# Optimization experiments

Measured on AMD Instinct MI355X. Metric: run time of the kernel, lower is better.

The kernel has to match this reference:

```python
import jax, jax.numpy as jnp
import numpy as np

EPS = 1e-5

def _bn_relu_over_batch(x, gamma, beta):
    # x: [..., B, F] where batch axis is -2; per-step training-mode BatchNorm1d
    mu = x.mean(axis=-2, keepdims=True)
    var = ((x - mu) ** 2).mean(axis=-2, keepdims=True)  # biased var (torch BN)
    xn = (x - mu) * jax.lax.rsqrt(var + EPS)
    return jax.nn.relu(xn * gamma + beta)

def setup_inputs() -> dict:
    key = jax.random.key(0)
    ks = jax.random.split(key, 8)
    B, T, D_in, E, C, D_out = 8192, 128, 2, 128, 128, 5
    s = 0.1
    return {
        "inputs": jax.random.normal(ks[0], (B, T, D_in), jnp.float32),
        "W_emb": jax.random.normal(ks[1], (E, D_in), jnp.float32) * s,
        "b_emb": jnp.zeros((E,), jnp.float32),
        "g_emb": jnp.ones((E,), jnp.float32),
        "be_emb": jnp.zeros((E,), jnp.float32),
        "W_ih": jax.random.normal(ks[2], (4 * C, E), jnp.float32) * s,
        "W_hh": jax.random.normal(ks[3], (4 * C, C), jnp.float32) * s,
        "b_ih": jnp.zeros((4 * C,), jnp.float32),
        "b_hh": jnp.zeros((4 * C,), jnp.float32),
        "W_out": jax.random.normal(ks[4], (D_out, C), jnp.float32) * s,
        "b_out": jnp.zeros((D_out,), jnp.float32),
        "g_out": jnp.ones((D_out,), jnp.float32),
        "be_out": jnp.zeros((D_out,), jnp.float32),
    }

def reference(inputs, W_emb, b_emb, g_emb, be_emb, W_ih, W_hh, b_ih, b_hh,
              W_out, b_out, g_out, be_out):
    B, T, _ = inputs.shape
    C = W_hh.shape[1]
    # Input embedding: Linear + per-step BatchNorm (batch stats) + ReLU, vectorized over T
    x = jnp.einsum('btd,ed->bte', inputs, W_emb) + b_emb      # [B,T,E]
    x = jnp.transpose(x, (1, 0, 2))                           # [T,B,E]
    x = _bn_relu_over_batch(x, g_emb, be_emb)                 # BN over batch per step

    def step(carry, xt):
        h, c = carry
        gates = xt @ W_ih.T + b_ih + h @ W_hh.T + b_hh        # [B,4C]
        i, f, g, o = jnp.split(gates, 4, axis=-1)             # torch LSTMCell order
        i = jax.nn.sigmoid(i); f = jax.nn.sigmoid(f)
        g = jnp.tanh(g); o = jax.nn.sigmoid(o)
        c = f * c + i * g
        h = o * jnp.tanh(c)
        return (h, c), h

    h0 = jnp.zeros((B, C), inputs.dtype)
    _, h_all = jax.lax.scan(step, (h0, h0), x)                # [T,B,C]

    # Output embedding: Linear + per-step BatchNorm + ReLU
    y = jnp.einsum('tbc,oc->tbo', h_all, W_out) + b_out       # [T,B,5]
    y = _bn_relu_over_batch(y, g_out, be_out)
    return jnp.transpose(y, (1, 0, 2))                        # [B,T,5]
```

## Files before the change

kernel.cpp:

```cpp
#include <hip/hip_runtime.h>

typedef __attribute__((ext_vector_type(8))) short short8;
typedef __attribute__((ext_vector_type(4))) float floatx4;

#define B_TOT 8192
#define T_STEPS 128
#define E_DIM 128
#define C_DIM 128
#define D_OUT 5
#define BN_EPS 1e-5f

#define LOG2E 1.4426950408889634f
#define TWO_LOG2E 2.8853900817779268f

#define WS_WCAT   0u
#define WS_WOUT   (WS_WCAT + 262144u)
#define WS_A0     (WS_WOUT + 4096u)
#define WS_A1     (WS_A0 + 65536u)
#define WS_CC     (WS_A1 + 65536u)
#define WS_STATS  (WS_CC + 65536u)
#define WS_PART   (WS_STATS + 5120u)
#define WS_Y      (WS_PART + 20480u)

__device__ __forceinline__ float bf2f(unsigned short h){
  return __uint_as_float(((unsigned int)h) << 16);
}
__device__ __forceinline__ unsigned short f2b(float v){
  unsigned int u = __float_as_uint(v);
  u += 0x7FFFu + ((u >> 16) & 1u);
  return (unsigned short)(u >> 16);
}
__device__ __forceinline__ unsigned short f2b_fast(float v){
  return (unsigned short)((__float_as_uint(v) + 0x8000u) >> 16);
}
__device__ __forceinline__ float ldf(const void* p, int i, int bf){
  return bf ? bf2f(((const unsigned short*)p)[i]) : ((const float*)p)[i];
}
__device__ __forceinline__ int sniff_bf(const void* ones){
  return *(const unsigned int*)ones == 0x3F803F80u;
}

__global__ void k_prep_mom(const void* W_ih, const void* W_hh, const void* W_out,
                           unsigned short* wcat, unsigned short* wout,
                           const void* x, float* part, const void* ones){
  const int bf = sniff_bf(ones);
  const int tid = threadIdx.x;
  if (blockIdx.x < 260){
    int i = blockIdx.x * 512 + tid;
    if (i < 512*256){
      int n = i >> 8, k = i & 255;
      float v = (k < 128) ? ldf(W_ih, n*128 + k, bf) : ldf(W_hh, n*128 + (k-128), bf);
      float sc = ((n >> 7) == 2) ? TWO_LOG2E : -LOG2E;
      wcat[i] = f2b(v * sc);
    } else {
      int j = i - 512*256;
      int n = j >> 7, k = j & 127;
      float v = (n < D_OUT) ? ldf(W_out, n*128 + k, bf) : 0.0f;
      wout[j] = f2b(v);
    }
    return;
  }
  const int mb  = blockIdx.x - 260;
  const int wdw = (mb >> 3) * 8;
  const int rg  = mb & 7;
  const int wv = tid >> 6, lane = tid & 63;
  __shared__ float red[8][16][3];

  if (!bf){
    const float* xp = (const float*)x;
    const int row_b = tid >> 4, j = tid & 15;
    float a0=0, a1=0, a2=0;
    for (int c = 0; c < 32; ++c){
      int row = rg*1024 + c*32 + row_b;
      float v = xp[row*256 + wdw*2 + j];
      float p = __shfl_xor(v, 1, 64);
      if ((j & 1) == 0){ a0 += v; a1 += v*v; a2 += v*p; }
      else             { a0 += v; a1 += v*v; }
    }
    a0 += __shfl_down(a0,32,64); a0 += __shfl_down(a0,16,64);
    a1 += __shfl_down(a1,32,64); a1 += __shfl_down(a1,16,64);
    a2 += __shfl_down(a2,32,64); a2 += __shfl_down(a2,16,64);
    if (lane < 16){ red[wv][lane][0]=a0; red[wv][lane][1]=a1; red[wv][lane][2]=a2; }
  } else {
    const unsigned int* xp = (const unsigned int*)x;
    const int row_b = tid >> 3, j = tid & 7;
    float s0=0,s1=0,s00=0,s11=0,s01=0;
    for (int c = 0; c < 16; ++c){
      int row = rg*1024 + c*64 + row_b;
      unsigned int u = xp[row*128 + wdw + j];
      float xv0 = bf2f((unsigned short)(u & 0xFFFFu));
      float xv1 = bf2f((unsigned short)(u >> 16));
      s0+=xv0; s1+=xv1; s00+=xv0*xv0; s11+=xv1*xv1; s01+=xv0*xv1;
    }
    s0 += __shfl_down(s0,32,64); s0 += __shfl_down(s0,16,64); s0 += __shfl_down(s0,8,64);
    s1 += __shfl_down(s1,32,64); s1 += __shfl_down(s1,16,64); s1 += __shfl_down(s1,8,64);
    s00+= __shfl_down(s00,32,64);s00+= __shfl_down(s00,16,64);s00+= __shfl_down(s00,8,64);
    s11+= __shfl_down(s11,32,64);s11+= __shfl_down(s11,16,64);s11+= __shfl_down(s11,8,64);
    s01+= __shfl_down(s01,32,64);s01+= __shfl_down(s01,16,64);s01+= __shfl_down(s01,8,64);
    if (lane < 8){
      red[wv][lane][0]=s0;  red[wv][lane][1]=s00; red[wv][lane][2]=s01;
      red[wv][8+lane][0]=s1; red[wv][8+lane][1]=s11;
    }
  }
  __syncthreads();
  if (tid < 8){
    int tl = tid;
    float S0=0,S1=0,S00=0,S11=0,S01=0;
    for (int w8 = 0; w8 < 8; ++w8){
      if (!bf){
        S0 += red[w8][2*tl][0];   S00 += red[w8][2*tl][1];   S01 += red[w8][2*tl][2];
        S1 += red[w8][2*tl+1][0]; S11 += red[w8][2*tl+1][1];
      } else {
        S0 += red[w8][tl][0];     S00 += red[w8][tl][1];     S01 += red[w8][tl][2];
        S1 += red[w8][8+tl][0];   S11 += red[w8][8+tl][1];
      }
    }
    float* dst = part + rg*640 + (wdw + tl)*5;
    dst[0]=S0; dst[1]=S1; dst[2]=S00; dst[3]=S11; dst[4]=S01;
  }
}

__global__ void k_coef(const float* part, const void* W_emb, const void* g_emb, const void* be_emb,
                       float* A0, float* A1, float* Cc){
  const int bf = sniff_bf(g_emb);
  int i = blockIdx.x*256 + threadIdx.x;
  int t = i >> 7, e = i & 127;
  float S0=0,S1=0,S00=0,S11=0,S01=0;
  for (int rg = 0; rg < 8; ++rg){
    const float* p = part + rg*640 + t*5;
    S0+=p[0]; S1+=p[1]; S00+=p[2]; S11+=p[3]; S01+=p[4];
  }
  const float inv = 1.0f / (float)B_TOT;
  float mu0 = S0*inv, mu1 = S1*inv;
  float v00 = S00*inv - mu0*mu0, v11 = S11*inv - mu1*mu1, c01 = S01*inv - mu0*mu1;
  float w0 = ldf(W_emb, e*2, bf), w1 = ldf(W_emb, e*2+1, bf);
  float g  = ldf(g_emb, e, bf),  be = ldf(be_emb, e, bf);
  float var = w0*w0*v00 + 2.0f*w0*w1*c01 + w1*w1*v11;
  float rs = rsqrtf(var + BN_EPS);
  float a0 = g*rs*w0, a1 = g*rs*w1;
  A0[i] = a0; A1[i] = a1;
  Cc[i] = be - (a0*mu0 + a1*mu1);
}

__global__ __launch_bounds__(512, 2)
void k_lstm(const void* x, const void* b_ih, const void* b_hh, const void* ones,
            const unsigned short* __restrict__ wcat, const unsigned short* __restrict__ wout,
            const float* __restrict__ A0, const float* __restrict__ A1, const float* __restrict__ Cc,
            float* __restrict__ y_ws){
  const int bf = sniff_bf(ones);
  const int tid = threadIdx.x;
  const int wid = tid >> 6, lane = tid & 63;
  const int q = lane >> 4, s = lane & 15;
  const int row0 = blockIdx.x * 32;

  __shared__ unsigned short xh[2][32][264];

  {
    short8 z;
#pragma unroll
    for (int j = 0; j < 8; ++j) z[j] = 0;
    unsigned short* base = &xh[0][0][0];
    for (int i = tid*8; i < 2*32*264; i += 512*8)
      *(short8*)(base + i) = z;
  }

  short8 bfr[4][8];
#pragma unroll
  for (int gq = 0; gq < 4; ++gq)
#pragma unroll
    for (int ks = 0; ks < 8; ++ks)
      bfr[gq][ks] = *(const short8*)(wcat + ((wid + 8*gq)*16 + s)*256 + ks*32 + q*8);

  short8 wf[4];
#pragma unroll
  for (int ks = 0; ks < 4; ++ks)
    wf[ks] = *(const short8*)(wout + s*128 + ks*32 + q*8);

  const int ch = 16*wid + s;
  floatx4 binit[4];
#pragma unroll
  for (int gq = 0; gq < 4; ++gq){
    float braw = ldf(b_ih, gq*128 + ch, bf) + ldf(b_hh, gq*128 + ch, bf);
    float b = braw * ((gq == 2) ? TWO_LOG2E : -LOG2E);
    binit[gq] = (floatx4){b, b, b, b};
  }

  float c_st[2][4] = {{0,0,0,0},{0,0,0,0}};

  const int r_loc = tid >> 4;
  const int e0 = (tid & 15) * 8;

  auto compute_xe = [&](int tt, int buf){
    float x0, x1;
    int xbase = ((row0 + r_loc)*T_STEPS + tt)*2;
    if (bf){ const unsigned short* xp = (const unsigned short*)x;
      x0 = bf2f(xp[xbase]); x1 = bf2f(xp[xbase+1]);
    } else { const float* xp = (const float*)x; x0 = xp[xbase]; x1 = xp[xbase+1]; }
    floatx4 a0a = *(const floatx4*)(A0 + tt*E_DIM + e0);
    floatx4 a0b = *(const floatx4*)(A0 + tt*E_DIM + e0 + 4);
    floatx4 a1a = *(const floatx4*)(A1 + tt*E_DIM + e0);
    floatx4 a1b = *(const floatx4*)(A1 + tt*E_DIM + e0 + 4);
    floatx4 cca = *(const floatx4*)(Cc + tt*E_DIM + e0);
    floatx4 ccb = *(const floatx4*)(Cc + tt*E_DIM + e0 + 4);
    short8 pack;
#pragma unroll
    for (int j = 0; j < 4; ++j){
      float v  = fmaxf(fmaf(a0a[j], x0, fmaf(a1a[j], x1, cca[j])), 0.0f);
      float v2 = fmaxf(fmaf(a0b[j], x0, fmaf(a1b[j], x1, ccb[j])), 0.0f);
      pack[j]   = (short)f2b_fast(v);
      pack[4+j] = (short)f2b_fast(v2);
    }
    *(short8*)&xh[buf][r_loc][e0] = pack;
  };

  __syncthreads();
  compute_xe(0, 0);
  __syncthreads();

  for (int t = 0; t < T_STEPS; ++t){
    const int cb = t & 1, nb = cb ^ 1;

    if (wid < 2 && t > 0){
      floatx4 ya = {0,0,0,0};
#pragma unroll
      for (int ks = 0; ks < 4; ++ks){
        short8 a = *(const short8*)&xh[cb][s + 16*wid][128 + ks*32 + q*8];
        ya = __builtin_amdgcn_mfma_f32_16x16x32_bf16(a, wf[ks], ya, 0, 0, 0);
      }
      if (s < D_OUT){
#pragma unroll
        for (int r = 0; r < 4; ++r){
          int row = row0 + 16*wid + q*4 + r;
          y_ws[((t-1)*B_TOT + row)*D_OUT + s] = ya[r];
        }
      }
    }

    floatx4 acc[2][4];
#pragma unroll
    for (int mt = 0; mt < 2; ++mt)
#pragma unroll
      for (int gq = 0; gq < 4; ++gq) acc[mt][gq] = binit[gq];
#pragma unroll
    for (int ks = 0; ks < 8; ++ks){
      short8 a0 = *(const short8*)&xh[cb][s][ks*32 + q*8];
      short8 a1 = *(const short8*)&xh[cb][s + 16][ks*32 + q*8];
#pragma unroll
      for (int gq = 0; gq < 4; ++gq){
        acc[0][gq] = __builtin_amdgcn_mfma_f32_16x16x32_bf16(a0, bfr[gq][ks], acc[0][gq], 0, 0, 0);
        acc[1][gq] = __builtin_amdgcn_mfma_f32_16x16x32_bf16(a1, bfr[gq][ks], acc[1][gq], 0, 0, 0);
      }
    }

#pragma unroll
    for (int mt = 0; mt < 2; ++mt){
#pragma unroll
      for (int r = 0; r < 4; ++r){
        float ea = __builtin_amdgcn_exp2f(fminf(acc[mt][0][r], 40.0f));
        float eb = __builtin_amdgcn_exp2f(fminf(acc[mt][1][r], 40.0f));
        float ec = __builtin_amdgcn_exp2f(fminf(acc[mt][2][r], 40.0f));
        float ed = __builtin_amdgcn_exp2f(fminf(acc[mt][3][r], 40.0f));
        float Aa = 1.0f + ea, Bb = 1.0f + eb, Ca = 1.0f + ec;
        float t1 = Aa * Ca;
        float r1 = __builtin_amdgcn_rcpf(t1 * Bb);
        float cn = fmaf(t1 * r1, c_st[mt][r], (Bb * r1) * (ec - 1.0f));
        c_st[mt][r] = cn;
        float E  = __builtin_amdgcn_exp2f(fminf(cn * TWO_LOG2E, 80.0f));
        float r2 = __builtin_amdgcn_rcpf((1.0f + ed) * (E + 1.0f));
        float hv = (E - 1.0f) * r2;
        xh[nb][16*mt + q*4 + r][128 + ch] = f2b_fast(hv);
      }
    }

    if (t < T_STEPS-1) compute_xe(t+1, nb);
    __syncthreads();
  }

  if (wid < 2){
    floatx4 ya = {0,0,0,0};
#pragma unroll
    for (int ks = 0; ks < 4; ++ks){
      short8 a = *(const short8*)&xh[0][s + 16*wid][128 + ks*32 + q*8];
      ya = __builtin_amdgcn_mfma_f32_16x16x32_bf16(a, wf[ks], ya, 0, 0, 0);
    }
    if (s < D_OUT){
#pragma unroll
      for (int r = 0; r < 4; ++r){
        int row = row0 + 16*wid + q*4 + r;
        y_ws[((T_STEPS-1)*B_TOT + row)*D_OUT + s] = ya[r];
      }
    }
  }
  asm volatile("s_waitcnt vmcnt(0)" ::: "memory");
}

__global__ void k_outstats(const float* __restrict__ y_ws, const void* g_out, const void* be_out,
                           float* stats, const void* ones){
  const int bf = sniff_bf(ones);
  const int t = blockIdx.x, tid = threadIdx.x;
  __shared__ float acc2[5][2];
  if (tid < 10) ((float*)acc2)[tid] = 0.0f;
  __syncthreads();
  float s[5] = {0,0,0,0,0}, ss[5] = {0,0,0,0,0};
  const float* base = y_ws + (size_t)t * 40960;
#pragma unroll 5
  for (int it = 0; it < 160; ++it){
    float v = base[it*256 + tid];
    s[it % 5] += v; ss[it % 5] += v*v;
  }
  int ob = tid % 5;
#pragma unroll
  for (int p = 0; p < 5; ++p){
    int o = ob + p; if (o >= 5) o -= 5;
    atomicAdd(&acc2[o][0], s[p]);
    atomicAdd(&acc2[o][1], ss[p]);
  }
  __syncthreads();
  if (tid < 5){
    float S = acc2[tid][0], SS = acc2[tid][1];
    const float inv = 1.0f / (float)B_TOT;
    float mu = S*inv, var = SS*inv - mu*mu;
    float g = ldf(g_out, tid, bf), be = ldf(be_out, tid, bf);
    float sc = g * rsqrtf(var + BN_EPS);
    stats[(t*5+tid)*2]   = sc;
    stats[(t*5+tid)*2+1] = be - sc*mu;
  }
}

__global__ void k_apply(const float* __restrict__ y_ws, const float* __restrict__ stats,
                        void* out, const void* ones){
  const int bf = sniff_bf(ones);
  __shared__ float tile[128*85];
  const int b0 = blockIdx.x * 16;
  const int tid = threadIdx.x;
  for (int i = tid; i < 10240; i += 256){
    int t = i / 80, j = i - t*80;
    tile[t*85 + j] = y_ws[((size_t)t*B_TOT + b0)*D_OUT + j];
  }
  __syncthreads();
  for (int i = tid; i < 10240; i += 256){
    int b = i / 640, r = i - b*640;
    int t = r / 5, o = r - t*5;
    float v = tile[t*85 + b*5 + o];
    v = fmaxf(fmaf(v, stats[r*2], stats[r*2+1]), 0.0f);
    int oi = b0*640 + i;
    if (bf) ((unsigned short*)out)[oi] = f2b(v);
    else    ((float*)out)[oi] = v;
  }
}

extern "C" void kernel_launch(void* const* d_in, const int* in_sizes, int n_in,
                              void* d_out, int out_size, void* d_ws, size_t ws_size,
                              hipStream_t stream){
  const void* x      = d_in[0];
  const void* W_emb  = d_in[1];
  const void* g_emb  = d_in[3];
  const void* be_emb = d_in[4];
  const void* W_ih   = d_in[5];
  const void* W_hh   = d_in[6];
  const void* b_ih   = d_in[7];
  const void* b_hh   = d_in[8];
  const void* W_out  = d_in[9];
  const void* g_out  = d_in[11];
  const void* be_out = d_in[12];

  char* ws = (char*)d_ws;
  unsigned short* wcat = (unsigned short*)(ws + WS_WCAT);
  unsigned short* wout = (unsigned short*)(ws + WS_WOUT);
  float* A0    = (float*)(ws + WS_A0);
  float* A1    = (float*)(ws + WS_A1);
  float* Cc    = (float*)(ws + WS_CC);
  float* stats = (float*)(ws + WS_STATS);
  float* part  = (float*)(ws + WS_PART);
  float* y_ws  = (float*)(ws + WS_Y);

  k_prep_mom<<<dim3(388),  dim3(512), 0, stream>>>(W_ih, W_hh, W_out, wcat, wout, x, part, g_emb);
  k_coef    <<<dim3(64),   dim3(256), 0, stream>>>(part, W_emb, g_emb, be_emb, A0, A1, Cc);
  k_lstm    <<<dim3(256),  dim3(512), 0, stream>>>(x, b_ih, b_hh, g_emb, wcat, wout, A0, A1, Cc, y_ws);
  k_outstats<<<dim3(128),  dim3(256), 0, stream>>>(y_ws, g_out, be_out, stats, g_emb);
  k_apply   <<<dim3(512),  dim3(256), 0, stream>>>(y_ws, stats, d_out, g_emb);
}
```

Before: 426.1 us.

## Fuse output BN partial stats into LSTM kernel via shared-memory y buffering

The LSTM kernel now buffers its output projections in shared memory for 32 timesteps. It flushes them in coalesced chunks and also writes per-workgroup partial sums and squared sums for the output BatchNorm. This replaces the k_outstats pass over y_ws with a small k_finstats reduction over 256 partials, and k_apply now stages the stats in LDS. The next-step embedding compute is moved ahead of the gate MFMAs, which may help overlap. The costs are about 20KB of extra LDS per block, which can hurt occupancy at 2 blocks per CU, and periodic flush stalls inside the serial recurrence.

```diff
diff --git a/kernel.cpp b/kernel.cpp
--- a/kernel.cpp
+++ b/kernel.cpp
@@ -18,9 +18,10 @@
 #define WS_A0     (WS_WOUT + 4096u)
 #define WS_A1     (WS_A0 + 65536u)
 #define WS_CC     (WS_A1 + 65536u)
-#define WS_STATS  (WS_CC + 65536u)
-#define WS_PART   (WS_STATS + 5120u)
-#define WS_Y      (WS_PART + 20480u)
+#define WS_PART   (WS_CC + 65536u)
+#define WS_PARTY  (WS_PART + 20480u)
+#define WS_STATS  (WS_PARTY + 1310720u)
+#define WS_Y      (WS_STATS + 5120u)
 
 __device__ __forceinline__ float bf2f(unsigned short h){
   return __uint_as_float(((unsigned int)h) << 16);
@@ -146,14 +147,16 @@
 void k_lstm(const void* x, const void* b_ih, const void* b_hh, const void* ones,
             const unsigned short* __restrict__ wcat, const unsigned short* __restrict__ wout,
             const float* __restrict__ A0, const float* __restrict__ A1, const float* __restrict__ Cc,
-            float* __restrict__ y_ws){
+            float* __restrict__ y_ws, float* __restrict__ part_y){
   const int bf = sniff_bf(ones);
   const int tid = threadIdx.x;
   const int wid = tid >> 6, lane = tid & 63;
   const int q = lane >> 4, s = lane & 15;
   const int row0 = blockIdx.x * 32;
+  const int wg = blockIdx.x;
 
   __shared__ unsigned short xh[2][32][264];
+  __shared__ float ybuf[32][32][5];
 
   {
     short8 z;
@@ -213,12 +216,32 @@
     *(short8*)&xh[buf][r_loc][e0] = pack;
   };
 
+  auto flush_chunk = [&](int c){
+    for (int i = tid; i < 5120; i += 512){
+      int slot = i >> 7;
+      slot = i / 160; int rem = i - slot*160;
+      y_ws[(size_t)(32*c + slot)*40960 + row0*5 + rem] = (&ybuf[slot][0][0])[rem];
+    }
+    if (tid < 160){
+      int tl = tid / 5, o = tid - (tid/5)*5;
+      float sm = 0.0f, sq = 0.0f;
+#pragma unroll 8
+      for (int r = 0; r < 32; ++r){ float v = ybuf[tl][r][o]; sm += v; sq += v*v; }
+      int pr = (32*c + tl)*5 + o;
+      part_y[(size_t)pr*256 + wg] = sm;
+      part_y[640u*256 + (size_t)pr*256 + wg] = sq;
+    }
+    __syncthreads();
+  };
+
   __syncthreads();
   compute_xe(0, 0);
   __syncthreads();
 
   for (int t = 0; t < T_STEPS; ++t){
     const int cb = t & 1, nb = cb ^ 1;
+
+    if (t >= 33 && ((t - 1) & 31) == 0) flush_chunk((t >> 5) - 1);
 
     if (wid < 2 && t > 0){
       floatx4 ya = {0,0,0,0};
@@ -229,12 +252,12 @@
       }
       if (s < D_OUT){
 #pragma unroll
-        for (int r = 0; r < 4; ++r){
-          int row = row0 + 16*wid + q*4 + r;
-          y_ws[((t-1)*B_TOT + row)*D_OUT + s] = ya[r];
-        }
-      }
-    }
+        for (int r = 0; r < 4; ++r)
+          ybuf[(t-1) & 31][16*wid + q*4 + r][s] = ya[r];
+      }
+    }
+
+    if (t < T_STEPS-1) compute_xe(t+1, nb);
 
     floatx4 acc[2][4];
 #pragma unroll
@@ -272,7 +295,6 @@
       }
     }
 
-    if (t < T_STEPS-1) compute_xe(t+1, nb);
     __syncthreads();
   }
 
@@ -285,54 +307,40 @@
     }
     if (s < D_OUT){
 #pragma unroll
-      for (int r = 0; r < 4; ++r){
-        int row = row0 + 16*wid + q*4 + r;
-        y_ws[((T_STEPS-1)*B_TOT + row)*D_OUT + s] = ya[r];
-      }
-    }
-  }
+      for (int r = 0; r < 4; ++r)
+        ybuf[31][16*wid + q*4 + r][s] = ya[r];
+    }
+  }
+  __syncthreads();
+  flush_chunk(3);
   asm volatile("s_waitcnt vmcnt(0)" ::: "memory");
 }
 
-__global__ void k_outstats(const float* __restrict__ y_ws, const void* g_out, const void* be_out,
-                           float* stats, const void* ones){
-  const int bf = sniff_bf(ones);
-  const int t = blockIdx.x, tid = threadIdx.x;
-  __shared__ float acc2[5][2];
-  if (tid < 10) ((float*)acc2)[tid] = 0.0f;
-  __syncthreads();
-  float s[5] = {0,0,0,0,0}, ss[5] = {0,0,0,0,0};
-  const float* base = y_ws + (size_t)t * 40960;
-#pragma unroll 5
-  for (int it = 0; it < 160; ++it){
-    float v = base[it*256 + tid];
-    s[it % 5] += v; ss[it % 5] += v*v;
-  }
-  int ob = tid % 5;
-#pragma unroll
-  for (int p = 0; p < 5; ++p){
-    int o = ob + p; if (o >= 5) o -= 5;
-    atomicAdd(&acc2[o][0], s[p]);
-    atomicAdd(&acc2[o][1], ss[p]);
-  }
-  __syncthreads();
-  if (tid < 5){
-    float S = acc2[tid][0], SS = acc2[tid][1];
-    const float inv = 1.0f / (float)B_TOT;
-    float mu = S*inv, var = SS*inv - mu*mu;
-    float g = ldf(g_out, tid, bf), be = ldf(be_out, tid, bf);
-    float sc = g * rsqrtf(var + BN_EPS);
-    stats[(t*5+tid)*2]   = sc;
-    stats[(t*5+tid)*2+1] = be - sc*mu;
-  }
+__global__ void k_finstats(const float* __restrict__ part_y, const void* g_out, const void* be_out,
+                           float* stats){
+  const int bf = sniff_bf(g_out);
+  int p = blockIdx.x*128 + threadIdx.x;
+  float S = 0.0f, SS = 0.0f;
+  const float* ps = part_y + (size_t)p*256;
+  const float* pq = part_y + 640u*256 + (size_t)p*256;
+  for (int w = 0; w < 256; ++w){ S += ps[w]; SS += pq[w]; }
+  const float inv = 1.0f / (float)B_TOT;
+  float mu = S*inv, var = SS*inv - mu*mu;
+  int o = p % 5;
+  float g = ldf(g_out, o, bf), be = ldf(be_out, o, bf);
+  float sc = g * rsqrtf(var + BN_EPS);
+  stats[2*p]   = sc;
+  stats[2*p+1] = be - sc*mu;
 }
 
 __global__ void k_apply(const float* __restrict__ y_ws, const float* __restrict__ stats,
                         void* out, const void* ones){
   const int bf = sniff_bf(ones);
   __shared__ float tile[128*85];
+  __shared__ float sstat[1280];
   const int b0 = blockIdx.x * 16;
   const int tid = threadIdx.x;
+  for (int i = tid; i < 1280; i += 256) sstat[i] = stats[i];
   for (int i = tid; i < 10240; i += 256){
     int t = i / 80, j = i - t*80;
     tile[t*85 + j] = y_ws[((size_t)t*B_TOT + b0)*D_OUT + j];
@@ -342,7 +350,7 @@
     int b = i / 640, r = i - b*640;
     int t = r / 5, o = r - t*5;
     float v = tile[t*85 + b*5 + o];
-    v = fmaxf(fmaf(v, stats[r*2], stats[r*2+1]), 0.0f);
+    v = fmaxf(fmaf(v, sstat[r*2], sstat[r*2+1]), 0.0f);
     int oi = b0*640 + i;
     if (bf) ((unsigned short*)out)[oi] = f2b(v);
     else    ((float*)out)[oi] = v;
@@ -367,16 +375,17 @@
   char* ws = (char*)d_ws;
   unsigned short* wcat = (unsigned short*)(ws + WS_WCAT);
   unsigned short* wout = (unsigned short*)(ws + WS_WOUT);
-  float* A0    = (float*)(ws + WS_A0);
-  float* A1    = (float*)(ws + WS_A1);
-  float* Cc    = (float*)(ws + WS_CC);
-  float* stats = (float*)(ws + WS_STATS);
-  float* part  = (float*)(ws + WS_PART);
-  float* y_ws  = (float*)(ws + WS_Y);
-
-  k_prep_mom<<<dim3(388),  dim3(512), 0, stream>>>(W_ih, W_hh, W_out, wcat, wout, x, part, g_emb);
-  k_coef    <<<dim3(64),   dim3(256), 0, stream>>>(part, W_emb, g_emb, be_emb, A0, A1, Cc);
-  k_lstm    <<<dim3(256),  dim3(512), 0, stream>>>(x, b_ih, b_hh, g_emb, wcat, wout, A0, A1, Cc, y_ws);
-  k_outstats<<<dim3(128),  dim3(256), 0, stream>>>(y_ws, g_out, be_out, stats, g_emb);
-  k_apply   <<<dim3(512),  dim3(256), 0, stream>>>(y_ws, stats, d_out, g_emb);
-}
+  float* A0     = (float*)(ws + WS_A0);
+  float* A1     = (float*)(ws + WS_A1);
+  float* Cc     = (float*)(ws + WS_CC);
+  float* part   = (float*)(ws + WS_PART);
+  float* part_y = (float*)(ws + WS_PARTY);
+  float* stats  = (float*)(ws + WS_STATS);
+  float* y_ws   = (float*)(ws + WS_Y);
+
+  k_prep_mom<<<dim3(388), dim3(512), 0, stream>>>(W_ih, W_hh, W_out, wcat, wout, x, part, g_emb);
+  k_coef    <<<dim3(64),  dim3(256), 0, stream>>>(part, W_emb, g_emb, be_emb, A0, A1, Cc);
+  k_lstm    <<<dim3(256), dim3(512), 0, stream>>>(x, b_ih, b_hh, g_emb, wcat, wout, A0, A1, Cc, y_ws, part_y);
+  k_finstats<<<dim3(5),   dim3(128), 0, stream>>>(part_y, g_out, be_out, stats);
+  k_apply   <<<dim3(512), dim3(256), 0, stream>>>(y_ws, stats, d_out, g_emb);
+}
```

Result: slower. 458.9 us (+7.7%).

## Fuse BN coefficient kernel into prep via last-block atomic; split LSTM MFMA chains

Applied to the files above, without the earlier changes.

The separate k_coef launch is removed. The last block of k_prep_mom to finish, found through an atomic counter with threadfences, now computes the embedding BN coefficients, which saves one kernel launch at the cost of a memset and a serial tail run by a single block. In the LSTM loop the two M-tiles are now issued as separate MFMA chains, each followed by its own cell update, which may let the first tile's activation math overlap the second tile's MFMAs. The y output address is also computed once and advanced by a pointer increment each step.

```diff
diff --git a/kernel.cpp b/kernel.cpp
--- a/kernel.cpp
+++ b/kernel.cpp
@@ -20,7 +20,8 @@
 #define WS_CC     (WS_A1 + 65536u)
 #define WS_STATS  (WS_CC + 65536u)
 #define WS_PART   (WS_STATS + 5120u)
-#define WS_Y      (WS_PART + 20480u)
+#define WS_CNT    (WS_PART + 20480u)
+#define WS_Y      (WS_CNT + 256u)
 
 __device__ __forceinline__ float bf2f(unsigned short h){
   return __uint_as_float(((unsigned int)h) << 16);
@@ -42,8 +43,10 @@
 
 __global__ void k_prep_mom(const void* W_ih, const void* W_hh, const void* W_out,
                            unsigned short* wcat, unsigned short* wout,
-                           const void* x, float* part, const void* ones){
-  const int bf = sniff_bf(ones);
+                           const void* x, float* part, unsigned int* cnt,
+                           const void* W_emb, const void* g_emb, const void* be_emb,
+                           float* A0, float* A1, float* Cc){
+  const int bf = sniff_bf(g_emb);
   const int tid = threadIdx.x;
   if (blockIdx.x < 260){
     int i = blockIdx.x * 512 + tid;
@@ -58,88 +61,94 @@
       float v = (n < D_OUT) ? ldf(W_out, n*128 + k, bf) : 0.0f;
       wout[j] = f2b(v);
     }
-    return;
-  }
-  const int mb  = blockIdx.x - 260;
-  const int wdw = (mb >> 3) * 8;
-  const int rg  = mb & 7;
-  const int wv = tid >> 6, lane = tid & 63;
-  __shared__ float red[8][16][3];
-
-  if (!bf){
-    const float* xp = (const float*)x;
-    const int row_b = tid >> 4, j = tid & 15;
-    float a0=0, a1=0, a2=0;
-    for (int c = 0; c < 32; ++c){
-      int row = rg*1024 + c*32 + row_b;
-      float v = xp[row*256 + wdw*2 + j];
-      float p = __shfl_xor(v, 1, 64);
-      if ((j & 1) == 0){ a0 += v; a1 += v*v; a2 += v*p; }
-      else             { a0 += v; a1 += v*v; }
-    }
-    a0 += __shfl_down(a0,32,64); a0 += __shfl_down(a0,16,64);
-    a1 += __shfl_down(a1,32,64); a1 += __shfl_down(a1,16,64);
-    a2 += __shfl_down(a2,32,64); a2 += __shfl_down(a2,16,64);
-    if (lane < 16){ red[wv][lane][0]=a0; red[wv][lane][1]=a1; red[wv][lane][2]=a2; }
   } else {
-    const unsigned int* xp = (const unsigned int*)x;
-    const int row_b = tid >> 3, j = tid & 7;
-    float s0=0,s1=0,s00=0,s11=0,s01=0;
-    for (int c = 0; c < 16; ++c){
-      int row = rg*1024 + c*64 + row_b;
-      unsigned int u = xp[row*128 + wdw + j];
-      float xv0 = bf2f((unsigned short)(u & 0xFFFFu));
-      float xv1 = bf2f((unsigned short)(u >> 16));
-      s0+=xv0; s1+=xv1; s00+=xv0*xv0; s11+=xv1*xv1; s01+=xv0*xv1;
-    }
-    s0 += __shfl_down(s0,32,64); s0 += __shfl_down(s0,16,64); s0 += __shfl_down(s0,8,64);
-    s1 += __shfl_down(s1,32,64); s1 += __shfl_down(s1,16,64); s1 += __shfl_down(s1,8,64);
-    s00+= __shfl_down(s00,32,64);s00+= __shfl_down(s00,16,64);s00+= __shfl_down(s00,8,64);
-    s11+= __shfl_down(s11,32,64);s11+= __shfl_down(s11,16,64);s11+= __shfl_down(s11,8,64);
-    s01+= __shfl_down(s01,32,64);s01+= __shfl_down(s01,16,64);s01+= __shfl_down(s01,8,64);
-    if (lane < 8){
-      red[wv][lane][0]=s0;  red[wv][lane][1]=s00; red[wv][lane][2]=s01;
-      red[wv][8+lane][0]=s1; red[wv][8+lane][1]=s11;
-    }
-  }
-  __syncthreads();
-  if (tid < 8){
-    int tl = tid;
-    float S0=0,S1=0,S00=0,S11=0,S01=0;
-    for (int w8 = 0; w8 < 8; ++w8){
-      if (!bf){
-        S0 += red[w8][2*tl][0];   S00 += red[w8][2*tl][1];   S01 += red[w8][2*tl][2];
-        S1 += red[w8][2*tl+1][0]; S11 += red[w8][2*tl+1][1];
-      } else {
-        S0 += red[w8][tl][0];     S00 += red[w8][tl][1];     S01 += red[w8][tl][2];
-        S1 += red[w8][8+tl][0];   S11 += red[w8][8+tl][1];
-      }
-    }
-    float* dst = part + rg*640 + (wdw + tl)*5;
-    dst[0]=S0; dst[1]=S1; dst[2]=S00; dst[3]=S11; dst[4]=S01;
-  }
-}
-
-__global__ void k_coef(const float* part, const void* W_emb, const void* g_emb, const void* be_emb,
-                       float* A0, float* A1, float* Cc){
-  const int bf = sniff_bf(g_emb);
-  int i = blockIdx.x*256 + threadIdx.x;
-  int t = i >> 7, e = i & 127;
-  float S0=0,S1=0,S00=0,S11=0,S01=0;
-  for (int rg = 0; rg < 8; ++rg){
-    const float* p = part + rg*640 + t*5;
-    S0+=p[0]; S1+=p[1]; S00+=p[2]; S11+=p[3]; S01+=p[4];
-  }
-  const float inv = 1.0f / (float)B_TOT;
-  float mu0 = S0*inv, mu1 = S1*inv;
-  float v00 = S00*inv - mu0*mu0, v11 = S11*inv - mu1*mu1, c01 = S01*inv - mu0*mu1;
-  float w0 = ldf(W_emb, e*2, bf), w1 = ldf(W_emb, e*2+1, bf);
-  float g  = ldf(g_emb, e, bf),  be = ldf(be_emb, e, bf);
-  float var = w0*w0*v00 + 2.0f*w0*w1*c01 + w1*w1*v11;
-  float rs = rsqrtf(var + BN_EPS);
-  float a0 = g*rs*w0, a1 = g*rs*w1;
-  A0[i] = a0; A1[i] = a1;
-  Cc[i] = be - (a0*mu0 + a1*mu1);
+    const int mb  = blockIdx.x - 260;
+    const int wdw = (mb >> 3) * 8;
+    const int rg  = mb & 7;
+    const int wv = tid >> 6, lane = tid & 63;
+    __shared__ float red[8][16][3];
+
+    if (!bf){
+      const float* xp = (const float*)x;
+      const int row_b = tid >> 4, j = tid & 15;
+      float a0=0, a1=0, a2=0;
+      for (int c = 0; c < 32; ++c){
+        int row = rg*1024 + c*32 + row_b;
+        float v = xp[row*256 + wdw*2 + j];
+        float p = __shfl_xor(v, 1, 64);
+        if ((j & 1) == 0){ a0 += v; a1 += v*v; a2 += v*p; }
+        else             { a0 += v; a1 += v*v; }
+      }
+      a0 += __shfl_down(a0,32,64); a0 += __shfl_down(a0,16,64);
+      a1 += __shfl_down(a1,32,64); a1 += __shfl_down(a1,16,64);
+      a2 += __shfl_down(a2,32,64); a2 += __shfl_down(a2,16,64);
+      if (lane < 16){ red[wv][lane][0]=a0; red[wv][lane][1]=a1; red[wv][lane][2]=a2; }
+    } else {
+      const unsigned int* xp = (const unsigned int*)x;
+      const int row_b = tid >> 3, j = tid & 7;
+      float s0=0,s1=0,s00=0,s11=0,s01=0;
+      for (int c = 0; c < 16; ++c){
+        int row = rg*1024 + c*64 + row_b;
+        unsigned int u = xp[row*128 + wdw + j];
+        float xv0 = bf2f((unsigned short)(u & 0xFFFFu));
+        float xv1 = bf2f((unsigned short)(u >> 16));
+        s0+=xv0; s1+=xv1; s00+=xv0*xv0; s11+=xv1*xv1; s01+=xv0*xv1;
+      }
+      s0 += __shfl_down(s0,32,64); s0 += __shfl_down(s0,16,64); s0 += __shfl_down(s0,8,64);
+      s1 += __shfl_down(s1,32,64); s1 += __shfl_down(s1,16,64); s1 += __shfl_down(s1,8,64);
+      s00+= __shfl_down(s00,32,64);s00+= __shfl_down(s00,16,64);s00+= __shfl_down(s00,8,64);
+      s11+= __shfl_down(s11,32,64);s11+= __shfl_down(s11,16,64);s11+= __shfl_down(s11,8,64);
+      s01+= __shfl_down(s01,32,64);s01+= __shfl_down(s01,16,64);s01+= __shfl_down(s01,8,64);
+      if (lane < 8){
+        red[wv][lane][0]=s0;  red[wv][lane][1]=s00; red[wv][lane][2]=s01;
+        red[wv][8+lane][0]=s1; red[wv][8+lane][1]=s11;
+      }
+    }
+    __syncthreads();
+    if (tid < 8){
+      int tl = tid;
+      float S0=0,S1=0,S00=0,S11=0,S01=0;
+      for (int w8 = 0; w8 < 8; ++w8){
+        if (!bf){
+          S0 += red[w8][2*tl][0];   S00 += red[w8][2*tl][1];   S01 += red[w8][2*tl][2];
+          S1 += red[w8][2*tl+1][0]; S11 += red[w8][2*tl+1][1];
+        } else {
+          S0 += red[w8][tl][0];     S00 += red[w8][tl][1];     S01 += red[w8][tl][2];
+          S1 += red[w8][8+tl][0];   S11 += red[w8][8+tl][1];
+        }
+      }
+      float* dst = part + rg*640 + (wdw + tl)*5;
+      dst[0]=S0; dst[1]=S1; dst[2]=S00; dst[3]=S11; dst[4]=S01;
+    }
+  }
+
+  __threadfence();
+  __shared__ unsigned int prior;
+  __syncthreads();
+  if (tid == 0) prior = atomicAdd(cnt, 1u);
+  __syncthreads();
+  if (prior == 387u){
+    __threadfence();
+    for (int i = tid; i < 128*128; i += 512){
+      int t = i >> 7, e = i & 127;
+      float S0=0,S1=0,S00=0,S11=0,S01=0;
+      for (int rg = 0; rg < 8; ++rg){
+        const float* p = part + rg*640 + t*5;
+        S0+=p[0]; S1+=p[1]; S00+=p[2]; S11+=p[3]; S01+=p[4];
+      }
+      const float inv = 1.0f / (float)B_TOT;
+      float mu0 = S0*inv, mu1 = S1*inv;
+      float v00 = S00*inv - mu0*mu0, v11 = S11*inv - mu1*mu1, c01 = S01*inv - mu0*mu1;
+      float w0 = ldf(W_emb, e*2, bf), w1 = ldf(W_emb, e*2+1, bf);
+      float g  = ldf(g_emb, e, bf),  be = ldf(be_emb, e, bf);
+      float var = w0*w0*v00 + 2.0f*w0*w1*c01 + w1*w1*v11;
+      float rs = rsqrtf(var + BN_EPS);
+      float a0 = g*rs*w0, a1 = g*rs*w1;
+      A0[i] = a0; A1[i] = a1;
+      Cc[i] = be - (a0*mu0 + a1*mu1);
+    }
+    __threadfence();
+  }
 }
 
 __global__ __launch_bounds__(512, 2)
@@ -213,6 +222,27 @@
     *(short8*)&xh[buf][r_loc][e0] = pack;
   };
 
+  auto cell_update = [&](floatx4* acc, int mt, int nb){
+#pragma unroll
+    for (int r = 0; r < 4; ++r){
+      float ea = __builtin_amdgcn_exp2f(fminf(acc[0][r], 40.0f));
+      float eb = __builtin_amdgcn_exp2f(fminf(acc[1][r], 40.0f));
+      float ec = __builtin_amdgcn_exp2f(fminf(acc[2][r], 40.0f));
+      float ed = __builtin_amdgcn_exp2f(fminf(acc[3][r], 40.0f));
+      float Aa = 1.0f + ea, Bb = 1.0f + eb, Ca = 1.0f + ec;
+      float t1 = Aa * Ca;
+      float r1 = __builtin_amdgcn_rcpf(t1 * Bb);
+      float cn = fmaf(t1 * r1, c_st[mt][r], (Bb * r1) * (ec - 1.0f));
+      c_st[mt][r] = cn;
+      float E  = __builtin_amdgcn_exp2f(fminf(cn * TWO_LOG2E, 80.0f));
+      float r2 = __builtin_amdgcn_rcpf((1.0f + ed) * (E + 1.0f));
+      float hv = (E - 1.0f) * r2;
+      xh[nb][16*mt + q*4 + r][128 + ch] = f2b_fast(hv);
+    }
+  };
+
+  float* ycur = y_ws + (row0 + 16*wid + q*4)*5 + s;
+
   __syncthreads();
   compute_xe(0, 0);
   __syncthreads();
@@ -229,48 +259,32 @@
       }
       if (s < D_OUT){
 #pragma unroll
-        for (int r = 0; r < 4; ++r){
-          int row = row0 + 16*wid + q*4 + r;
-          y_ws[((t-1)*B_TOT + row)*D_OUT + s] = ya[r];
-        }
-      }
-    }
-
-    floatx4 acc[2][4];
-#pragma unroll
-    for (int mt = 0; mt < 2; ++mt)
-#pragma unroll
-      for (int gq = 0; gq < 4; ++gq) acc[mt][gq] = binit[gq];
+        for (int r = 0; r < 4; ++r)
+          ycur[r*5] = ya[r];
+      }
+      ycur += 40960;
+    }
+
+    floatx4 acc0[4], acc1[4];
+#pragma unroll
+    for (int gq = 0; gq < 4; ++gq){ acc0[gq] = binit[gq]; acc1[gq] = binit[gq]; }
 #pragma unroll
     for (int ks = 0; ks < 8; ++ks){
       short8 a0 = *(const short8*)&xh[cb][s][ks*32 + q*8];
+#pragma unroll
+      for (int gq = 0; gq < 4; ++gq)
+        acc0[gq] = __builtin_amdgcn_mfma_f32_16x16x32_bf16(a0, bfr[gq][ks], acc0[gq], 0, 0, 0);
+    }
+#pragma unroll
+    for (int ks = 0; ks < 8; ++ks){
       short8 a1 = *(const short8*)&xh[cb][s + 16][ks*32 + q*8];
 #pragma unroll
-      for (int gq = 0; gq < 4; ++gq){
-        acc[0][gq] = __builtin_amdgcn_mfma_f32_16x16x32_bf16(a0, bfr[gq][ks], acc[0][gq], 0, 0, 0);
-        acc[1][gq] = __builtin_amdgcn_mfma_f32_16x16x32_bf16(a1, bfr[gq][ks], acc[1][gq], 0, 0, 0);
-      }
-    }
-
-#pragma unroll
-    for (int mt = 0; mt < 2; ++mt){
-#pragma unroll
-      for (int r = 0; r < 4; ++r){
-        float ea = __builtin_amdgcn_exp2f(fminf(acc[mt][0][r], 40.0f));
-        float eb = __builtin_amdgcn_exp2f(fminf(acc[mt][1][r], 40.0f));
-        float ec = __builtin_amdgcn_exp2f(fminf(acc[mt][2][r], 40.0f));
-        float ed = __builtin_amdgcn_exp2f(fminf(acc[mt][3][r], 40.0f));
-        float Aa = 1.0f + ea, Bb = 1.0f + eb, Ca = 1.0f + ec;
-        float t1 = Aa * Ca;
-        float r1 = __builtin_amdgcn_rcpf(t1 * Bb);
-        float cn = fmaf(t1 * r1, c_st[mt][r], (Bb * r1) * (ec - 1.0f));
-        c_st[mt][r] = cn;
-        float E  = __builtin_amdgcn_exp2f(fminf(cn * TWO_LOG2E, 80.0f));
-        float r2 = __builtin_amdgcn_rcpf((1.0f + ed) * (E + 1.0f));
-        float hv = (E - 1.0f) * r2;
-        xh[nb][16*mt + q*4 + r][128 + ch] = f2b_fast(hv);
-      }
-    }
+      for (int gq = 0; gq < 4; ++gq)
+        acc1[gq] = __builtin_amdgcn_mfma_f32_16x16x32_bf16(a1, bfr[gq][ks], acc1[gq], 0, 0, 0);
+    }
+
+    cell_update(acc0, 0, nb);
+    cell_update(acc1, 1, nb);
 
     if (t < T_STEPS-1) compute_xe(t+1, nb);
     __syncthreads();
@@ -285,10 +299,8 @@
     }
     if (s < D_OUT){
 #pragma unroll
-      for (int r = 0; r < 4; ++r){
-        int row = row0 + 16*wid + q*4 + r;
-        y_ws[((T_STEPS-1)*B_TOT + row)*D_OUT + s] = ya[r];
-      }
+      for (int r = 0; r < 4; ++r)
+        ycur[r*5] = ya[r];
     }
   }
   asm volatile("s_waitcnt vmcnt(0)" ::: "memory");
@@ -372,10 +384,13 @@
   float* Cc    = (float*)(ws + WS_CC);
   float* stats = (float*)(ws + WS_STATS);
   float* part  = (float*)(ws + WS_PART);
+  unsigned int* cnt = (unsigned int*)(ws + WS_CNT);
   float* y_ws  = (float*)(ws + WS_Y);
 
-  k_prep_mom<<<dim3(388),  dim3(512), 0, stream>>>(W_ih, W_hh, W_out, wcat, wout, x, part, g_emb);
-  k_coef    <<<dim3(64),   dim3(256), 0, stream>>>(part, W_emb, g_emb, be_emb, A0, A1, Cc);
+  hipMemsetAsync((void*)cnt, 0, 4, stream);
+  k_prep_mom<<<dim3(388),  dim3(512), 0, stream>>>(W_ih, W_hh, W_out, wcat, wout,
+                                                   x, part, cnt,
+                                                   W_emb, g_emb, be_emb, A0, A1, Cc);
   k_lstm    <<<dim3(256),  dim3(512), 0, stream>>>(x, b_ih, b_hh, g_emb, wcat, wout, A0, A1, Cc, y_ws);
   k_outstats<<<dim3(128),  dim3(256), 0, stream>>>(y_ws, g_out, be_out, stats, g_emb);
   k_apply   <<<dim3(512),  dim3(256), 0, stream>>>(y_ws, stats, d_out, g_emb);
```

After: 515.9 us. +21.1%, slower.
